# Kernel tuning notes

Hardware: AMD Instinct MI355X
Metric: run time of the kernel (lower is better)

The kernel has to match this reference:

```python
import jax, jax.numpy as jnp
import numpy as np
from math import sqrt

B, H, N, DK, ED = 8, 8, 1024, 64, 16


def setup_inputs() -> dict:
    key = jax.random.key(0)
    ks = jax.random.split(key, 9)
    Q = jax.random.normal(ks[0], (B, H, N, DK), dtype=jnp.float32)
    K = jax.random.normal(ks[1], (B, H, N, DK), dtype=jnp.float32)
    V = jax.random.normal(ks[2], (B, H, N, DK), dtype=jnp.float32)
    attn_mask = jax.random.randint(ks[3], (B, 1, N, N), 0, 2) > 0
    edge_feat = jax.random.normal(ks[4], (B, N, N, ED), dtype=jnp.float32)
    # edge-bias MLP params: Linear(ED, DK) -> Tanh -> Linear(DK, 1)
    W1 = jax.random.normal(ks[5], (ED, DK), dtype=jnp.float32) / sqrt(ED)
    b1 = jnp.zeros((DK,), dtype=jnp.float32)
    W2 = jax.random.normal(ks[6], (DK, 1), dtype=jnp.float32) / sqrt(DK)
    b2 = jnp.zeros((1,), dtype=jnp.float32)
    return {"Q": Q, "K": K, "V": V, "attn_mask": attn_mask,
            "edge_feat": edge_feat, "W1": W1, "b1": b1, "W2": W2, "b2": b2}


def reference(Q, K, V, attn_mask, edge_feat, W1, b1, W2, b2):
    d_k = Q.shape[-1]
    # scores: [B,H,N,N]
    scores = jnp.einsum('bhqd,bhkd->bhqk', Q, K) / jnp.sqrt(jnp.float32(d_k))
    # edge bias MLP: [B,N,N,ED] -> [B,N,N,1] -> squeeze(-1).unsqueeze(1) -> [B,1,N,N]
    h = jnp.tanh(jnp.einsum('bqke,ed->bqkd', edge_feat, W1) + b1)
    bias = (jnp.einsum('bqkd,do->bqko', h, W2) + b2)[..., 0][:, None, :, :]
    scores = scores + bias
    scores = jnp.where(attn_mask, jnp.float32(-1e9), scores)
    attn = jax.nn.softmax(scores, axis=-1)
    # dropout p=0.0 -> identity
    context = jnp.einsum('bhqk,bhkd->bhqd', attn, V)
    return (context, attn)
```

## Files before the change

kernel.cpp:

```cpp
#include <hip/hip_runtime.h>
#include <stdint.h>

constexpr int NB = 8, NH = 8, NN = 1024, DK = 64, ED = 16;
constexpr long QSZ = (long)NB * NH * NN * DK;

typedef _Float16 h8 __attribute__((ext_vector_type(8)));
typedef _Float16 h4 __attribute__((ext_vector_type(4)));
typedef _Float16 h2 __attribute__((ext_vector_type(2)));
typedef float f4 __attribute__((ext_vector_type(4)));
typedef float fv16 __attribute__((ext_vector_type(16)));

constexpr size_t OFF_QH = 0;
constexpr size_t OFF_KH = 8388608;
constexpr size_t OFF_VT = 16777216;
constexpr size_t OFF_BIAS = 25165824;
constexpr size_t OFF_FLAG = 58720256;
constexpr size_t WS_NEED = OFF_FLAG + 4;

constexpr float LG2E = 1.4426950408889634f;
constexpr float C2 = 2.8853900817779268f;
constexpr float QS = 0.125f * LG2E;

static __device__ __forceinline__ float fexp2(float x) {
  float r; asm("v_exp_f32 %0, %1" : "=v"(r) : "v"(x)); return r;
}
static __device__ __forceinline__ float frcp(float x) {
  float r; asm("v_rcp_f32 %0, %1" : "=v"(r) : "v"(x)); return r;
}
static __device__ __forceinline__ h2 pkrtz(float a, float b) {
  return __builtin_bit_cast(h2, __builtin_amdgcn_cvt_pkrtz(a, b));
}
static __device__ __forceinline__ void gl16(const void* g, void* l) {
  __builtin_amdgcn_global_load_lds(
      (const __attribute__((address_space(1))) uint32_t*)g,
      (__attribute__((address_space(3))) uint32_t*)l, 16, 0, 0);
}

__global__ __launch_bounds__(256) void k_prep_qk(
    const float* __restrict__ Q, const float* __restrict__ K,
    _Float16* __restrict__ Qh, _Float16* __restrict__ Kh) {
  int i = blockIdx.x * 256 + threadIdx.x;
  const int n4 = (int)(QSZ / 4);
  if (i < n4) {
    float4 v = reinterpret_cast<const float4*>(Q)[i];
    h4 o; o[0] = (_Float16)(v.x * QS); o[1] = (_Float16)(v.y * QS);
          o[2] = (_Float16)(v.z * QS); o[3] = (_Float16)(v.w * QS);
    reinterpret_cast<h4*>(Qh)[i] = o;
  } else {
    int j = i - n4;
    float4 v = reinterpret_cast<const float4*>(K)[j];
    h4 o; o[0] = (_Float16)v.x; o[1] = (_Float16)v.y;
          o[2] = (_Float16)v.z; o[3] = (_Float16)v.w;
    reinterpret_cast<h4*>(Kh)[j] = o;
  }
}

__global__ __launch_bounds__(256) void k_prep_vt(
    const float* __restrict__ V, _Float16* __restrict__ Vt) {
  int wid = (blockIdx.x * 256 + threadIdx.x) >> 6;
  int lane = threadIdx.x & 63;
  int bh = wid >> 6;
  int k0 = (wid & 63) << 4;
  const float* Vb = V + (long)bh * NN * DK;
  _Float16* Vo = Vt + (long)bh * DK * NN + (long)lane * NN + k0;
  h8 p0, p1;
#pragma unroll
  for (int i = 0; i < 16; ++i) {
    float v = Vb[(long)(k0 + i) * DK + lane];
    if (i < 8) p0[i] = (_Float16)v; else p1[i - 8] = (_Float16)v;
  }
  *reinterpret_cast<h8*>(Vo) = p0;
  *reinterpret_cast<h8*>(Vo + 8) = p1;
}

__global__ void k_detect(const unsigned char* __restrict__ m, int* __restrict__ flag) {
  __shared__ int sh[4];
  int t = threadIdx.x;
  int any = 0;
  for (int i = t; i < 4096; i += 256)
    if ((i & 3) && m[i]) any = 1;
  unsigned long long b = __ballot(any);
  if ((t & 63) == 0) sh[t >> 6] = (b != 0) ? 1 : 0;
  __syncthreads();
  if (t == 0) flag[0] = sh[0] | sh[1] | sh[2] | sh[3];
}

__global__ __launch_bounds__(256, 3) void k_bias(
    const float* __restrict__ edge, const void* __restrict__ maskp,
    const float* __restrict__ W1, const float* __restrict__ b1,
    const float* __restrict__ W2, const float* __restrict__ b2,
    const int* __restrict__ flag, _Float16* __restrict__ biasM) {
  int bq = blockIdx.x;
  int w = threadIdx.x >> 6, l = threadIdx.x & 63;
  int h = l >> 5, c31 = l & 31;
  bool isbool = (*flag != 0);
  h8 aw0, aw1;
#pragma unroll
  for (int j = 0; j < 8; ++j) {
    aw0[j] = (_Float16)(W1[(8 * h + j) * 64 + 0  + c31] * C2);
    aw1[j] = (_Float16)(W1[(8 * h + j) * 64 + 32 + c31] * C2);
  }
  h2 pb[16], pw[16];
  float sw = 0.f;
#pragma unroll
  for (int r = 0; r < 16; ++r) {
    int dr = (r & 3) + 8 * (r >> 2) + 4 * h;
    float b0 = b1[dr] * C2, b1v = b1[32 + dr] * C2;
    float w0 = W2[dr], w1v = W2[32 + dr];
    pb[r] = pkrtz(b0, b1v);
    pw[r] = pkrtz(w0, w1v);
    sw += w0 + w1v;
  }
  sw += __shfl_xor(sw, 32, 64);
  float base = (sw + b2[0]) * LG2E;

  const float* erow = edge + (long)bq * NN * ED;
  const float4* erow4 = reinterpret_cast<const float4*>(erow);
  _Float16* orow = biasM + (long)bq * NN;
  const int* mrowi = (const int*)maskp + (long)bq * NN;
  const unsigned char* mrowb = (const unsigned char*)maskp + (long)bq * NN;

  fv16 z;
#pragma unroll
  for (int r = 0; r < 16; ++r) z[r] = 0.f;

  int kbase = w * 256;
  float4 e0a = erow4[(kbase + c31) * 4 + 2 * h];
  float4 e0b = erow4[(kbase + c31) * 4 + 2 * h + 1];
  float4 e1a = erow4[(kbase + 32 + c31) * 4 + 2 * h];
  float4 e1b = erow4[(kbase + 32 + c31) * 4 + 2 * h + 1];
#pragma unroll
  for (int p = 0; p < 4; ++p) {
    float4 n0a, n0b, n1a, n1b;
    if (p < 3) {
      int nb = kbase + 64;
      n0a = erow4[(nb + c31) * 4 + 2 * h];
      n0b = erow4[(nb + c31) * 4 + 2 * h + 1];
      n1a = erow4[(nb + 32 + c31) * 4 + 2 * h];
      n1b = erow4[(nb + 32 + c31) * 4 + 2 * h + 1];
    }
    union { h8 v; h2 q[4]; } u0, u1;
    u0.q[0] = pkrtz(e0a.x, e0a.y); u0.q[1] = pkrtz(e0a.z, e0a.w);
    u0.q[2] = pkrtz(e0b.x, e0b.y); u0.q[3] = pkrtz(e0b.z, e0b.w);
    u1.q[0] = pkrtz(e1a.x, e1a.y); u1.q[1] = pkrtz(e1a.z, e1a.w);
    u1.q[2] = pkrtz(e1b.x, e1b.y); u1.q[3] = pkrtz(e1b.z, e1b.w);
    float a00 = 0.f, a01 = 0.f, a10 = 0.f, a11 = 0.f;
    {
      fv16 hA0 = __builtin_amdgcn_mfma_f32_32x32x16_f16(aw0, u0.v, z, 0, 0, 0);
      fv16 hA1 = __builtin_amdgcn_mfma_f32_32x32x16_f16(aw0, u1.v, z, 0, 0, 0);
#pragma unroll
      for (int r = 0; r < 16; ++r) {
        float bb = (float)pb[r][0];
        float ww = (float)pw[r][0];
        if (r & 1) {
          a01 = fmaf(ww, frcp(fexp2(hA0[r] + bb) + 1.f), a01);
          a11 = fmaf(ww, frcp(fexp2(hA1[r] + bb) + 1.f), a11);
        } else {
          a00 = fmaf(ww, frcp(fexp2(hA0[r] + bb) + 1.f), a00);
          a10 = fmaf(ww, frcp(fexp2(hA1[r] + bb) + 1.f), a10);
        }
      }
    }
    {
      fv16 hB0 = __builtin_amdgcn_mfma_f32_32x32x16_f16(aw1, u0.v, z, 0, 0, 0);
      fv16 hB1 = __builtin_amdgcn_mfma_f32_32x32x16_f16(aw1, u1.v, z, 0, 0, 0);
#pragma unroll
      for (int r = 0; r < 16; ++r) {
        float bb = (float)pb[r][1];
        float ww = (float)pw[r][1];
        if (r & 1) {
          a01 = fmaf(ww, frcp(fexp2(hB0[r] + bb) + 1.f), a01);
          a11 = fmaf(ww, frcp(fexp2(hB1[r] + bb) + 1.f), a11);
        } else {
          a00 = fmaf(ww, frcp(fexp2(hB0[r] + bb) + 1.f), a00);
          a10 = fmaf(ww, frcp(fexp2(hB1[r] + bb) + 1.f), a10);
        }
      }
    }
    float p0 = a00 + a01;
    float p1 = a10 + a11;
    p0 += __shfl_xor(p0, 32, 64);
    p1 += __shfl_xor(p1, 32, 64);
    float part = h ? p1 : p0;
    int idx = kbase + 32 * h + c31;
    int m = isbool ? (int)mrowb[idx] : mrowi[idx];
    orow[idx] = m ? (_Float16)(-30000.0f) : (_Float16)fmaf(-C2, part, base);
    e0a = n0a; e0b = n0b; e1a = n1a; e1b = n1b;
    kbase += 64;
  }
}

__global__ __launch_bounds__(256) void k_attn(
    const _Float16* __restrict__ Qh, const _Float16* __restrict__ Kh,
    const _Float16* __restrict__ Vt, const _Float16* __restrict__ biasH,
    float* __restrict__ ctx, float* __restrict__ attn) {
  int bid = blockIdx.x;
  int b = bid & 7;
  int t_ = bid >> 3;
  int hh = t_ & 7;
  int qb = t_ >> 3;
  int bh = b * 8 + hh;
  int tid = threadIdx.x;
  int w = tid >> 6, l = tid & 63;
  int g = l >> 4, s = l & 15;
  int q0 = qb * 64 + w * 16;

  const _Float16* Qw = Qh + ((long)bh * NN + q0) * DK;
  const char* Kbase = (const char*)(Kh + (long)bh * NN * DK);
  const char* Vbase = (const char*)(Vt + (long)bh * DK * NN);
  const char* Bbase = (const char*)(biasH + (long)b * NN * NN + (long)(qb * 64) * NN);
  h8 aQ0 = *reinterpret_cast<const h8*>(Qw + s * DK + 8 * g);
  h8 aQ1 = *reinterpret_cast<const h8*>(Qw + s * DK + 32 + 8 * g);
  const f4 z4 = {0.f, 0.f, 0.f, 0.f};

  __shared__ __align__(16) _Float16 kt[2][32 * 64];
  __shared__ __align__(16) _Float16 vt2[2][64 * 32];
  __shared__ __align__(16) _Float16 bt[2][64 * 32];
  __shared__ float pf[4][16][33];

  int krow = tid >> 3;
  int kcol = ((tid & 7) * 16) ^ ((krow & 7) << 4);
  int vrow = tid >> 2;
  int vcol = ((tid & 3) * 16) ^ ((vrow & 3) << 4);
  int brow = tid >> 2;
  int bcol = (tid & 3) * 16;
  int wofs = w << 10;

  int ksw = (s & 7) << 4;
  int vswz = (s & 3) << 4;

#define STK(buf, c0) gl16(Kbase + (long)((c0) + krow) * 128 + kcol, (char*)kt[buf] + wofs)
#define STV(buf, c0) gl16(Vbase + (long)vrow * 2048 + (c0) * 2 + vcol, (char*)vt2[buf] + wofs)
#define STB(buf, c0) gl16(Bbase + (long)brow * 2048 + (c0) * 2 + bcol, (char*)bt[buf] + wofs)
#define BIAS(buf, j, kvl) ((float)*(const _Float16*)((const char*)bt[buf] + (w * 16 + 4 * g + (j)) * 64 + (kvl) * 2))

  float ls0 = 0.f, ls1 = 0.f, ls2 = 0.f, ls3 = 0.f;
  STK(0, 0); STB(0, 0);
  {
    int buf = 0;
    for (int c0 = 0; c0 < NN; c0 += 32, buf ^= 1) {
      __syncthreads();
      if (c0 + 32 < NN) { STK(buf ^ 1, c0 + 32); STB(buf ^ 1, c0 + 32); }
      const char* kbuf = (const char*)kt[buf];
      h8 k0 = *(const h8*)(kbuf + s * 128 + ((16 * g) ^ ksw));
      h8 k1 = *(const h8*)(kbuf + s * 128 + ((64 + 16 * g) ^ ksw));
      f4 acc = __builtin_amdgcn_mfma_f32_16x16x32_f16(aQ0, k0, z4, 0, 0, 0);
      acc = __builtin_amdgcn_mfma_f32_16x16x32_f16(aQ1, k1, acc, 0, 0, 0);
      ls0 += fexp2(acc[0] + BIAS(buf, 0, s));
      ls1 += fexp2(acc[1] + BIAS(buf, 1, s));
      ls2 += fexp2(acc[2] + BIAS(buf, 2, s));
      ls3 += fexp2(acc[3] + BIAS(buf, 3, s));
      k0 = *(const h8*)(kbuf + (16 + s) * 128 + ((16 * g) ^ ksw));
      k1 = *(const h8*)(kbuf + (16 + s) * 128 + ((64 + 16 * g) ^ ksw));
      acc = __builtin_amdgcn_mfma_f32_16x16x32_f16(aQ0, k0, z4, 0, 0, 0);
      acc = __builtin_amdgcn_mfma_f32_16x16x32_f16(aQ1, k1, acc, 0, 0, 0);
      ls0 += fexp2(acc[0] + BIAS(buf, 0, 16 + s));
      ls1 += fexp2(acc[1] + BIAS(buf, 1, 16 + s));
      ls2 += fexp2(acc[2] + BIAS(buf, 2, 16 + s));
      ls3 += fexp2(acc[3] + BIAS(buf, 3, 16 + s));
    }
  }
#pragma unroll
  for (int m = 1; m < 16; m <<= 1) {
    ls0 += __shfl_xor(ls0, m, 64);
    ls1 += __shfl_xor(ls1, m, 64);
    ls2 += __shfl_xor(ls2, m, 64);
    ls3 += __shfl_xor(ls3, m, 64);
  }
  float iv0 = frcp(ls0), iv1 = frcp(ls1), iv2 = frcp(ls2), iv3 = frcp(ls3);

  f4 ca0 = {0.f,0.f,0.f,0.f}, ca1 = {0.f,0.f,0.f,0.f};
  f4 ca2 = {0.f,0.f,0.f,0.f}, ca3 = {0.f,0.f,0.f,0.f};
  float* attnw = attn + ((long)bh * NN + q0) * NN;
  int sr = l >> 3, sc = (l & 7) * 4;
  __syncthreads();
  STK(0, 0); STV(0, 0); STB(0, 0);
  {
    int buf = 0;
    for (int c0 = 0; c0 < NN; c0 += 32, buf ^= 1) {
      __syncthreads();
      if (c0 + 32 < NN) { STK(buf ^ 1, c0 + 32); STV(buf ^ 1, c0 + 32); STB(buf ^ 1, c0 + 32); }
      const char* kbuf = (const char*)kt[buf];
      const char* vbuf = (const char*)vt2[buf];
      h8 k0 = *(const h8*)(kbuf + s * 128 + ((16 * g) ^ ksw));
      h8 k1 = *(const h8*)(kbuf + s * 128 + ((64 + 16 * g) ^ ksw));
      f4 acc = __builtin_amdgcn_mfma_f32_16x16x32_f16(aQ0, k0, z4, 0, 0, 0);
      acc = __builtin_amdgcn_mfma_f32_16x16x32_f16(aQ1, k1, acc, 0, 0, 0);
      pf[w][4 * g + 0][s] = fexp2(acc[0] + BIAS(buf, 0, s)) * iv0;
      pf[w][4 * g + 1][s] = fexp2(acc[1] + BIAS(buf, 1, s)) * iv1;
      pf[w][4 * g + 2][s] = fexp2(acc[2] + BIAS(buf, 2, s)) * iv2;
      pf[w][4 * g + 3][s] = fexp2(acc[3] + BIAS(buf, 3, s)) * iv3;
      k0 = *(const h8*)(kbuf + (16 + s) * 128 + ((16 * g) ^ ksw));
      k1 = *(const h8*)(kbuf + (16 + s) * 128 + ((64 + 16 * g) ^ ksw));
      acc = __builtin_amdgcn_mfma_f32_16x16x32_f16(aQ0, k0, z4, 0, 0, 0);
      acc = __builtin_amdgcn_mfma_f32_16x16x32_f16(aQ1, k1, acc, 0, 0, 0);
      pf[w][4 * g + 0][16 + s] = fexp2(acc[0] + BIAS(buf, 0, 16 + s)) * iv0;
      pf[w][4 * g + 1][16 + s] = fexp2(acc[1] + BIAS(buf, 1, 16 + s)) * iv1;
      pf[w][4 * g + 2][16 + s] = fexp2(acc[2] + BIAS(buf, 2, 16 + s)) * iv2;
      pf[w][4 * g + 3][16 + s] = fexp2(acc[3] + BIAS(buf, 3, 16 + s)) * iv3;
      f4 row0 = *reinterpret_cast<const f4*>(&pf[w][sr][sc]);
      f4 row1 = *reinterpret_cast<const f4*>(&pf[w][sr + 8][sc]);
      *reinterpret_cast<f4*>(attnw + (long)sr * NN + c0 + sc) = row0;
      *reinterpret_cast<f4*>(attnw + (long)(sr + 8) * NN + c0 + sc) = row1;
      f4 pa = *reinterpret_cast<const f4*>(&pf[w][s][8 * g]);
      f4 pb4 = *reinterpret_cast<const f4*>(&pf[w][s][8 * g + 4]);
      union { h8 v; h2 q[4]; } up;
      up.q[0] = pkrtz(pa[0], pa[1]);  up.q[1] = pkrtz(pa[2], pa[3]);
      up.q[2] = pkrtz(pb4[0], pb4[1]); up.q[3] = pkrtz(pb4[2], pb4[3]);
      h8 aP = up.v;
      h8 bv0 = *(const h8*)(vbuf + (s)      * 64 + ((16 * g) ^ vswz));
      h8 bv1 = *(const h8*)(vbuf + (16 + s) * 64 + ((16 * g) ^ vswz));
      h8 bv2 = *(const h8*)(vbuf + (32 + s) * 64 + ((16 * g) ^ vswz));
      h8 bv3 = *(const h8*)(vbuf + (48 + s) * 64 + ((16 * g) ^ vswz));
      ca0 = __builtin_amdgcn_mfma_f32_16x16x32_f16(aP, bv0, ca0, 0, 0, 0);
      ca1 = __builtin_amdgcn_mfma_f32_16x16x32_f16(aP, bv1, ca1, 0, 0, 0);
      ca2 = __builtin_amdgcn_mfma_f32_16x16x32_f16(aP, bv2, ca2, 0, 0, 0);
      ca3 = __builtin_amdgcn_mfma_f32_16x16x32_f16(aP, bv3, ca3, 0, 0, 0);
    }
  }
  float* cw = ctx + ((long)bh * NN + q0) * DK;
#pragma unroll
  for (int j = 0; j < 4; ++j) {
    cw[(4 * g + j) * DK + 0  + s] = ca0[j];
    cw[(4 * g + j) * DK + 16 + s] = ca1[j];
    cw[(4 * g + j) * DK + 32 + s] = ca2[j];
    cw[(4 * g + j) * DK + 48 + s] = ca3[j];
  }
#undef STK
#undef STV
#undef STB
#undef BIAS
}

extern "C" void kernel_launch(void* const* d_in, const int* in_sizes, int n_in,
                              void* d_out, int out_size, void* d_ws, size_t ws_size,
                              hipStream_t stream) {
  const float* Q = (const float*)d_in[0];
  const float* K = (const float*)d_in[1];
  const float* V = (const float*)d_in[2];
  const void* mask = d_in[3];
  const float* edge = (const float*)d_in[4];
  const float* W1 = (const float*)d_in[5];
  const float* b1 = (const float*)d_in[6];
  const float* W2 = (const float*)d_in[7];
  const float* b2 = (const float*)d_in[8];
  float* ctx = (float*)d_out;
  float* attn = ctx + QSZ;
  char* ws = (char*)d_ws;
  if (ws_size < WS_NEED) return;
  _Float16* Qh = (_Float16*)(ws + OFF_QH);
  _Float16* Kh = (_Float16*)(ws + OFF_KH);
  _Float16* Vt = (_Float16*)(ws + OFF_VT);
  _Float16* biasM = (_Float16*)(ws + OFF_BIAS);
  int* flag = (int*)(ws + OFF_FLAG);

  k_detect<<<1, 256, 0, stream>>>((const unsigned char*)mask, flag);
  k_prep_qk<<<8192, 256, 0, stream>>>(Q, K, Qh, Kh);
  k_prep_vt<<<1024, 256, 0, stream>>>(V, Vt);
  k_bias<<<8192, 256, 0, stream>>>(edge, mask, W1, b1, W2, b2, flag, biasM);
  k_attn<<<1024, 256, 0, stream>>>(Qh, Kh, Vt, biasM, ctx, attn);
}
```

Measured before the change: 306.9 us.

## Stage edge features via LDS async loads and merge prep kernels

The edge-bias kernel no longer reads edge features with strided per-lane float4 global loads. It now stages each 64-row tile into a double-buffered, XOR-swizzled LDS buffer using global_load_lds, gated by vmcnt waits, then reads the MFMA operands from LDS. Mask loads are hoisted to the start and the bias stores are deferred to the end. The Q/K conversion and V transpose kernels are merged into one launch to save a kernel launch. The kernel now uses 32KB of static LDS per block, which may lower occupancy, and the correctness of the swizzle and wait counts must hold.

```diff
diff --git a/kernel.cpp b/kernel.cpp
--- a/kernel.cpp
+++ b/kernel.cpp
@@ -36,41 +36,41 @@
       (__attribute__((address_space(3))) uint32_t*)l, 16, 0, 0);
 }
 
-__global__ __launch_bounds__(256) void k_prep_qk(
-    const float* __restrict__ Q, const float* __restrict__ K,
-    _Float16* __restrict__ Qh, _Float16* __restrict__ Kh) {
-  int i = blockIdx.x * 256 + threadIdx.x;
-  const int n4 = (int)(QSZ / 4);
-  if (i < n4) {
-    float4 v = reinterpret_cast<const float4*>(Q)[i];
-    h4 o; o[0] = (_Float16)(v.x * QS); o[1] = (_Float16)(v.y * QS);
-          o[2] = (_Float16)(v.z * QS); o[3] = (_Float16)(v.w * QS);
-    reinterpret_cast<h4*>(Qh)[i] = o;
+__global__ __launch_bounds__(256) void k_prep(
+    const float* __restrict__ Q, const float* __restrict__ K, const float* __restrict__ V,
+    _Float16* __restrict__ Qh, _Float16* __restrict__ Kh, _Float16* __restrict__ Vt) {
+  int bid = blockIdx.x;
+  if (bid < 8192) {
+    int i = bid * 256 + threadIdx.x;
+    const int n4 = (int)(QSZ / 4);
+    if (i < n4) {
+      float4 v = reinterpret_cast<const float4*>(Q)[i];
+      h4 o; o[0] = (_Float16)(v.x * QS); o[1] = (_Float16)(v.y * QS);
+            o[2] = (_Float16)(v.z * QS); o[3] = (_Float16)(v.w * QS);
+      reinterpret_cast<h4*>(Qh)[i] = o;
+    } else {
+      int j = i - n4;
+      float4 v = reinterpret_cast<const float4*>(K)[j];
+      h4 o; o[0] = (_Float16)v.x; o[1] = (_Float16)v.y;
+            o[2] = (_Float16)v.z; o[3] = (_Float16)v.w;
+      reinterpret_cast<h4*>(Kh)[j] = o;
+    }
   } else {
-    int j = i - n4;
-    float4 v = reinterpret_cast<const float4*>(K)[j];
-    h4 o; o[0] = (_Float16)v.x; o[1] = (_Float16)v.y;
-          o[2] = (_Float16)v.z; o[3] = (_Float16)v.w;
-    reinterpret_cast<h4*>(Kh)[j] = o;
-  }
-}
-
-__global__ __launch_bounds__(256) void k_prep_vt(
-    const float* __restrict__ V, _Float16* __restrict__ Vt) {
-  int wid = (blockIdx.x * 256 + threadIdx.x) >> 6;
-  int lane = threadIdx.x & 63;
-  int bh = wid >> 6;
-  int k0 = (wid & 63) << 4;
-  const float* Vb = V + (long)bh * NN * DK;
-  _Float16* Vo = Vt + (long)bh * DK * NN + (long)lane * NN + k0;
-  h8 p0, p1;
-#pragma unroll
-  for (int i = 0; i < 16; ++i) {
-    float v = Vb[(long)(k0 + i) * DK + lane];
-    if (i < 8) p0[i] = (_Float16)v; else p1[i - 8] = (_Float16)v;
-  }
-  *reinterpret_cast<h8*>(Vo) = p0;
-  *reinterpret_cast<h8*>(Vo + 8) = p1;
+    int wid = ((bid - 8192) * 256 + threadIdx.x) >> 6;
+    int lane = threadIdx.x & 63;
+    int bh = wid >> 6;
+    int k0 = (wid & 63) << 4;
+    const float* Vb = V + (long)bh * NN * DK;
+    _Float16* Vo = Vt + (long)bh * DK * NN + (long)lane * NN + k0;
+    h8 p0, p1;
+#pragma unroll
+    for (int i = 0; i < 16; ++i) {
+      float v = Vb[(long)(k0 + i) * DK + lane];
+      if (i < 8) p0[i] = (_Float16)v; else p1[i - 8] = (_Float16)v;
+    }
+    *reinterpret_cast<h8*>(Vo) = p0;
+    *reinterpret_cast<h8*>(Vo + 8) = p1;
+  }
 }
 
 __global__ void k_detect(const unsigned char* __restrict__ m, int* __restrict__ flag) {
@@ -114,8 +114,7 @@
   sw += __shfl_xor(sw, 32, 64);
   float base = (sw + b2[0]) * LG2E;
 
-  const float* erow = edge + (long)bq * NN * ED;
-  const float4* erow4 = reinterpret_cast<const float4*>(erow);
+  const char* erow_b = (const char*)(edge + (long)bq * NN * ED);
   _Float16* orow = biasM + (long)bq * NN;
   const int* mrowi = (const int*)maskp + (long)bq * NN;
   const unsigned char* mrowb = (const unsigned char*)maskp + (long)bq * NN;
@@ -124,26 +123,44 @@
 #pragma unroll
   for (int r = 0; r < 16; ++r) z[r] = 0.f;
 
-  int kbase = w * 256;
-  float4 e0a = erow4[(kbase + c31) * 4 + 2 * h];
-  float4 e0b = erow4[(kbase + c31) * 4 + 2 * h + 1];
-  float4 e1a = erow4[(kbase + 32 + c31) * 4 + 2 * h];
-  float4 e1b = erow4[(kbase + 32 + c31) * 4 + 2 * h + 1];
+  int kq0 = w * 256;
+  int m4[4];
 #pragma unroll
   for (int p = 0; p < 4; ++p) {
-    float4 n0a, n0b, n1a, n1b;
-    if (p < 3) {
-      int nb = kbase + 64;
-      n0a = erow4[(nb + c31) * 4 + 2 * h];
-      n0b = erow4[(nb + c31) * 4 + 2 * h + 1];
-      n1a = erow4[(nb + 32 + c31) * 4 + 2 * h];
-      n1b = erow4[(nb + 32 + c31) * 4 + 2 * h + 1];
-    }
+    int idx = kq0 + p * 64 + 32 * h + c31;
+    m4[p] = isbool ? (int)mrowb[idx] : mrowi[idx];
+  }
+
+  __shared__ __align__(16) float ebuf[4][2][1024];
+  int r4 = l >> 2;
+  int csw = ((l & 3) * 16) ^ ((r4 & 3) << 4);
+#define STAGE(buf, p) do { \
+    const char* src_ = erow_b + (long)(kq0 + (p) * 64) * 64; \
+    char* dst_ = (char*)&ebuf[w][buf][0]; \
+    gl16(src_ + (long)(r4) * 64 + csw, dst_); \
+    gl16(src_ + (long)(16 + r4) * 64 + csw, dst_ + 1024); \
+    gl16(src_ + (long)(32 + r4) * 64 + csw, dst_ + 2048); \
+    gl16(src_ + (long)(48 + r4) * 64 + csw, dst_ + 3072); \
+  } while (0)
+
+  int sw0 = (c31 & 3) << 4;
+  float res[4];
+  STAGE(0, 0);
+#pragma unroll
+  for (int p = 0; p < 4; ++p) {
+    if (p < 3) STAGE((p + 1) & 1, p + 1);
+    if (p < 3) { asm volatile("s_waitcnt vmcnt(4)" ::: "memory"); }
+    else       { asm volatile("s_waitcnt vmcnt(0)" ::: "memory"); }
+    const char* tb = (const char*)&ebuf[w][p & 1][0];
+    f4 e0a = *(const f4*)(tb + c31 * 64 + ((h * 32) ^ sw0));
+    f4 e0b = *(const f4*)(tb + c31 * 64 + ((h * 32 + 16) ^ sw0));
+    f4 e1a = *(const f4*)(tb + (32 + c31) * 64 + ((h * 32) ^ sw0));
+    f4 e1b = *(const f4*)(tb + (32 + c31) * 64 + ((h * 32 + 16) ^ sw0));
     union { h8 v; h2 q[4]; } u0, u1;
-    u0.q[0] = pkrtz(e0a.x, e0a.y); u0.q[1] = pkrtz(e0a.z, e0a.w);
-    u0.q[2] = pkrtz(e0b.x, e0b.y); u0.q[3] = pkrtz(e0b.z, e0b.w);
-    u1.q[0] = pkrtz(e1a.x, e1a.y); u1.q[1] = pkrtz(e1a.z, e1a.w);
-    u1.q[2] = pkrtz(e1b.x, e1b.y); u1.q[3] = pkrtz(e1b.z, e1b.w);
+    u0.q[0] = pkrtz(e0a[0], e0a[1]); u0.q[1] = pkrtz(e0a[2], e0a[3]);
+    u0.q[2] = pkrtz(e0b[0], e0b[1]); u0.q[3] = pkrtz(e0b[2], e0b[3]);
+    u1.q[0] = pkrtz(e1a[0], e1a[1]); u1.q[1] = pkrtz(e1a[2], e1a[3]);
+    u1.q[2] = pkrtz(e1b[0], e1b[1]); u1.q[3] = pkrtz(e1b[2], e1b[3]);
     float a00 = 0.f, a01 = 0.f, a10 = 0.f, a11 = 0.f;
     {
       fv16 hA0 = __builtin_amdgcn_mfma_f32_32x32x16_f16(aw0, u0.v, z, 0, 0, 0);
@@ -181,12 +198,13 @@
     float p1 = a10 + a11;
     p0 += __shfl_xor(p0, 32, 64);
     p1 += __shfl_xor(p1, 32, 64);
-    float part = h ? p1 : p0;
-    int idx = kbase + 32 * h + c31;
-    int m = isbool ? (int)mrowb[idx] : mrowi[idx];
-    orow[idx] = m ? (_Float16)(-30000.0f) : (_Float16)fmaf(-C2, part, base);
-    e0a = n0a; e0b = n0b; e1a = n1a; e1b = n1b;
-    kbase += 64;
+    res[p] = h ? p1 : p0;
+  }
+#undef STAGE
+#pragma unroll
+  for (int p = 0; p < 4; ++p) {
+    int idx = kq0 + p * 64 + 32 * h + c31;
+    orow[idx] = m4[p] ? (_Float16)(-30000.0f) : (_Float16)fmaf(-C2, res[p], base);
   }
 }
 
@@ -355,8 +373,7 @@
   int* flag = (int*)(ws + OFF_FLAG);
 
   k_detect<<<1, 256, 0, stream>>>((const unsigned char*)mask, flag);
-  k_prep_qk<<<8192, 256, 0, stream>>>(Q, K, Qh, Kh);
-  k_prep_vt<<<1024, 256, 0, stream>>>(V, Vt);
+  k_prep<<<9216, 256, 0, stream>>>(Q, K, V, Qh, Kh, Vt);
   k_bias<<<8192, 256, 0, stream>>>(edge, mask, W1, b1, W2, b2, flag, biasM);
   k_attn<<<1024, 256, 0, stream>>>(Qh, Kh, Vt, biasM, ctx, attn);
 }
```

After: 303.0 us. About the same (-1.3%).
